# Kernel tuning notes

Measured on AMD Instinct MI355X. Metric: run time of the kernel, lower is better.

Reference implementation:

```python
import jax, jax.numpy as jnp
import numpy as np

N_AC = 8192     # number of amacrine cells
N_BC = 8192     # number of bipolar-cell helpers
T_KERNEL = 52   # len(torch.arange(0.8, 0, -1/64)) with input_frequency=64


def setup_inputs() -> dict:
    key = jax.random.key(0)
    k_x, k_w, k_k, k_s, k_o = jax.random.split(key, 5)
    x = jax.random.normal(k_x, (N_BC, T_KERNEL), dtype=jnp.float32)
    bc_ac_weight = jax.random.normal(k_w, (N_AC, N_BC), dtype=jnp.float32) / np.sqrt(N_BC)
    ac_kernel = jax.random.normal(k_k, (N_AC, T_KERNEL), dtype=jnp.float32)
    # normalize kernel rows like compute_ac_kernel does
    ac_kernel = ac_kernel / jnp.linalg.norm(ac_kernel, axis=1, keepdims=True)
    # slopes come from exp(log_slope) in the original -> keep positive
    ac_sigmoid_slope = jax.random.uniform(k_s, (N_AC,), dtype=jnp.float32) + 0.5
    ac_sigmoid_offset = 0.1 * jax.random.normal(k_o, (N_AC,), dtype=jnp.float32)
    return {
        "x": x,
        "bc_ac_weight": bc_ac_weight,
        "ac_kernel": ac_kernel,
        "ac_sigmoid_slope": ac_sigmoid_slope,
        "ac_sigmoid_offset": ac_sigmoid_offset,
    }


def reference(x, bc_ac_weight, ac_kernel, ac_sigmoid_slope, ac_sigmoid_offset):
    """One AC feedback step.

    x:                (nBC, T)   BC activity history window
    bc_ac_weight:     (nAC, nBC) precomputed (exp of log weights)
    ac_kernel:        (nAC, T)   precomputed normalized double-exp kernel
    ac_sigmoid_slope: (nAC,)
    ac_sigmoid_offset:(nAC,)
    returns:          (nAC,)
    """
    t_kernel = ac_kernel.shape[-1]
    y = bc_ac_weight @ x  # (nAC, T)
    if y.shape[-1] < t_kernel:  # static-shape left zero-pad as in F.pad
        y = jnp.pad(y, ((0, 0), (t_kernel - y.shape[-1], 0)))
    s = jnp.sum(ac_kernel * y, axis=1)  # temporal weighted sum -> (nAC,)
    # precomputed_sigmoid: sigmoid with per-cell slope and offset
    return jax.nn.sigmoid(ac_sigmoid_slope * (s - ac_sigmoid_offset))
```

## Files before the change

### kernel.cpp

```cpp
#include <hip/hip_runtime.h>
#include <hip/hip_bf16.h>
#include <math.h>

#define N_AC  8192
#define N_BC  8192
#define T_K   52
#define T_PAD 64

typedef __bf16 bf16x8 __attribute__((ext_vector_type(8)));
typedef float  f32x4  __attribute__((ext_vector_type(4)));

__global__ void xpose_kernel(const float* __restrict__ x, __bf16* __restrict__ xT) {
    int b = blockIdx.x * blockDim.x + threadIdx.x;
    if (b >= N_BC) return;
    #pragma unroll
    for (int t = 0; t < T_PAD; ++t) {
        float v = (t < T_K) ? x[b * T_K + t] : 0.0f;
        xT[(size_t)t * N_BC + b] = (__bf16)v;
    }
}

__global__ __launch_bounds__(256) void ac_feedback_kernel(
    const float*  __restrict__ W,
    const __bf16* __restrict__ xT,
    const float*  __restrict__ kern,
    const float*  __restrict__ slope,
    const float*  __restrict__ offs,
    float*        __restrict__ out)
{
    const int lane = threadIdx.x & 63;
    const int wave = threadIdx.x >> 6;
    const int quad = lane >> 4;
    const int l15  = lane & 15;
    const int a0   = blockIdx.x * 16;

    const float* wrow = W + (size_t)(a0 + l15) * N_BC;

    f32x4 acc[4] = {};

    const int kseg = N_BC / 4;
    const int kbeg = wave * kseg;
    const int koff = quad * 8;

    #pragma unroll 4
    for (int k = kbeg; k < kbeg + kseg; k += 32) {
        const float* wp = wrow + k + koff;
        float4 w0 = *(const float4*)(wp);
        float4 w1 = *(const float4*)(wp + 4);
        bf16x8 af;
        af[0] = (__bf16)w0.x; af[1] = (__bf16)w0.y;
        af[2] = (__bf16)w0.z; af[3] = (__bf16)w0.w;
        af[4] = (__bf16)w1.x; af[5] = (__bf16)w1.y;
        af[6] = (__bf16)w1.z; af[7] = (__bf16)w1.w;
        #pragma unroll
        for (int nt = 0; nt < 4; ++nt) {
            bf16x8 bf = *(const bf16x8*)(xT + (size_t)(nt * 16 + l15) * N_BC + k + koff);
            acc[nt] = __builtin_amdgcn_mfma_f32_16x16x32_bf16(af, bf, acc[nt], 0, 0, 0);
        }
    }

    float p[4] = {0.f, 0.f, 0.f, 0.f};
    #pragma unroll
    for (int nt = 0; nt < 4; ++nt) {
        int t = nt * 16 + l15;
        if (t < T_K) {
            #pragma unroll
            for (int r = 0; r < 4; ++r) {
                int grow = a0 + quad * 4 + r;
                p[r] += acc[nt][r] * kern[grow * T_K + t];
            }
        }
    }

    #pragma unroll
    for (int m = 1; m <= 8; m <<= 1) {
        #pragma unroll
        for (int r = 0; r < 4; ++r) p[r] += __shfl_xor(p[r], m);
    }

    __shared__ float red[4][16];
    if (l15 == 0) {
        #pragma unroll
        for (int r = 0; r < 4; ++r) red[wave][quad * 4 + r] = p[r];
    }
    __syncthreads();

    if (threadIdx.x < 16) {
        int a = a0 + threadIdx.x;
        float s = red[0][threadIdx.x] + red[1][threadIdx.x]
                + red[2][threadIdx.x] + red[3][threadIdx.x];
        float z = slope[a] * (s - offs[a]);
        out[a] = 1.0f / (1.0f + __expf(-z));
    }
}

extern "C" void kernel_launch(void* const* d_in, const int* in_sizes, int n_in,
                              void* d_out, int out_size, void* d_ws, size_t ws_size,
                              hipStream_t stream) {
    const float* x     = (const float*)d_in[0];
    const float* W     = (const float*)d_in[1];
    const float* kern  = (const float*)d_in[2];
    const float* slope = (const float*)d_in[3];
    const float* offs  = (const float*)d_in[4];
    float* out = (float*)d_out;

    __bf16* xT = (__bf16*)d_ws;

    xpose_kernel<<<dim3(N_BC / 256), dim3(256), 0, stream>>>(x, xT);
    ac_feedback_kernel<<<dim3(N_AC / 16), dim3(256), 0, stream>>>(
        W, xT, kern, slope, offs, out);
}
```

Baseline: 397.5 us.

## Split K across blocks and stage W tiles through LDS with coalesced loads

The GEMM kernel now uses a 2D grid that splits the reduction dimension into four segments, one per block. Each block loads 16x512 tiles of W with fully coalesced float4 loads, converts them to bf16, and stores them in padded shared memory before running the MFMAs. Partial sums go to a workspace buffer, and a new final kernel adds them and applies the sigmoid. This aims to improve W streaming coalescing and raise block-level parallelism, at the cost of an extra launch, a partials buffer, and barriers with no double buffering.

Result: slower. 433.7 us (+9.1%).

```diff
diff --git a/kernel.cpp b/kernel.cpp
--- a/kernel.cpp
+++ b/kernel.cpp
@@ -7,7 +7,14 @@
 #define T_K   52
 #define T_PAD 64
 
+#define KSPLIT 4
+#define KSEG   (N_BC / KSPLIT)
+#define BK     512
+#define NCHUNK (KSEG / BK)
+#define LDS_STRIDE 520
+
 typedef __bf16 bf16x8 __attribute__((ext_vector_type(8)));
+typedef __bf16 bf16x4 __attribute__((ext_vector_type(4)));
 typedef float  f32x4  __attribute__((ext_vector_type(4)));
 
 __global__ void xpose_kernel(const float* __restrict__ x, __bf16* __restrict__ xT) {
@@ -20,43 +27,54 @@
     }
 }
 
-__global__ __launch_bounds__(256) void ac_feedback_kernel(
+__global__ __launch_bounds__(256) void ac_gemm_kernel(
     const float*  __restrict__ W,
     const __bf16* __restrict__ xT,
     const float*  __restrict__ kern,
-    const float*  __restrict__ slope,
-    const float*  __restrict__ offs,
-    float*        __restrict__ out)
+    float*        __restrict__ partials)
 {
-    const int lane = threadIdx.x & 63;
-    const int wave = threadIdx.x >> 6;
+    const int tid  = threadIdx.x;
+    const int lane = tid & 63;
+    const int wave = tid >> 6;
     const int quad = lane >> 4;
     const int l15  = lane & 15;
     const int a0   = blockIdx.x * 16;
+    const int kbase = blockIdx.y * KSEG;
 
-    const float* wrow = W + (size_t)(a0 + l15) * N_BC;
+    __shared__ __bf16 As[16 * LDS_STRIDE];
 
     f32x4 acc[4] = {};
 
-    const int kseg = N_BC / 4;
-    const int kbeg = wave * kseg;
     const int koff = quad * 8;
+    const int ks   = wave * (BK / 4);
 
-    #pragma unroll 4
-    for (int k = kbeg; k < kbeg + kseg; k += 32) {
-        const float* wp = wrow + k + koff;
-        float4 w0 = *(const float4*)(wp);
-        float4 w1 = *(const float4*)(wp + 4);
-        bf16x8 af;
-        af[0] = (__bf16)w0.x; af[1] = (__bf16)w0.y;
-        af[2] = (__bf16)w0.z; af[3] = (__bf16)w0.w;
-        af[4] = (__bf16)w1.x; af[5] = (__bf16)w1.y;
-        af[6] = (__bf16)w1.z; af[7] = (__bf16)w1.w;
+    for (int c = 0; c < NCHUNK; ++c) {
+        const int kc = kbase + c * BK;
+
         #pragma unroll
-        for (int nt = 0; nt < 4; ++nt) {
-            bf16x8 bf = *(const bf16x8*)(xT + (size_t)(nt * 16 + l15) * N_BC + k + koff);
-            acc[nt] = __builtin_amdgcn_mfma_f32_16x16x32_bf16(af, bf, acc[nt], 0, 0, 0);
+        for (int j = 0; j < 8; ++j) {
+            int idx4 = j * 256 + tid;
+            int row  = idx4 >> 7;
+            int col  = (idx4 & 127) << 2;
+            float4 f = *(const float4*)(W + (size_t)(a0 + row) * N_BC + kc + col);
+            bf16x4 h;
+            h[0] = (__bf16)f.x; h[1] = (__bf16)f.y;
+            h[2] = (__bf16)f.z; h[3] = (__bf16)f.w;
+            *(bf16x4*)&As[row * LDS_STRIDE + col] = h;
         }
+        __syncthreads();
+
+        #pragma unroll
+        for (int s = 0; s < 4; ++s) {
+            int kk = ks + s * 32 + koff;
+            bf16x8 af = *(const bf16x8*)&As[l15 * LDS_STRIDE + kk];
+            #pragma unroll
+            for (int nt = 0; nt < 4; ++nt) {
+                bf16x8 bf = *(const bf16x8*)(xT + (size_t)(nt * 16 + l15) * N_BC + kc + kk);
+                acc[nt] = __builtin_amdgcn_mfma_f32_16x16x32_bf16(af, bf, acc[nt], 0, 0, 0);
+            }
+        }
+        __syncthreads();
     }
 
     float p[4] = {0.f, 0.f, 0.f, 0.f};
@@ -71,7 +89,6 @@
             }
         }
     }
-
     #pragma unroll
     for (int m = 1; m <= 8; m <<= 1) {
         #pragma unroll
@@ -85,13 +102,22 @@
     }
     __syncthreads();
 
-    if (threadIdx.x < 16) {
-        int a = a0 + threadIdx.x;
-        float s = red[0][threadIdx.x] + red[1][threadIdx.x]
-                + red[2][threadIdx.x] + red[3][threadIdx.x];
-        float z = slope[a] * (s - offs[a]);
-        out[a] = 1.0f / (1.0f + __expf(-z));
+    if (tid < 16) {
+        float s = red[0][tid] + red[1][tid] + red[2][tid] + red[3][tid];
+        partials[blockIdx.y * N_AC + a0 + tid] = s;
     }
+}
+
+__global__ void ac_final_kernel(const float* __restrict__ partials,
+                                const float* __restrict__ slope,
+                                const float* __restrict__ offs,
+                                float* __restrict__ out) {
+    int a = blockIdx.x * blockDim.x + threadIdx.x;
+    if (a >= N_AC) return;
+    float s = partials[a] + partials[N_AC + a]
+            + partials[2 * N_AC + a] + partials[3 * N_AC + a];
+    float z = slope[a] * (s - offs[a]);
+    out[a] = 1.0f / (1.0f + __expf(-z));
 }
 
 extern "C" void kernel_launch(void* const* d_in, const int* in_sizes, int n_in,
@@ -104,9 +130,12 @@
     const float* offs  = (const float*)d_in[4];
     float* out = (float*)d_out;
 
-    __bf16* xT = (__bf16*)d_ws;
+    __bf16* xT      = (__bf16*)d_ws;
+    float* partials = (float*)((char*)d_ws + (size_t)T_PAD * N_BC * sizeof(__bf16));
 
     xpose_kernel<<<dim3(N_BC / 256), dim3(256), 0, stream>>>(x, xT);
-    ac_feedback_kernel<<<dim3(N_AC / 16), dim3(256), 0, stream>>>(
-        W, xT, kern, slope, offs, out);
+    ac_gemm_kernel<<<dim3(N_AC / 16, KSPLIT), dim3(256), 0, stream>>>(
+        W, xT, kern, partials);
+    ac_final_kernel<<<dim3(N_AC / 256), dim3(256), 0, stream>>>(
+        partials, slope, offs, out);
 }
```

## Split GEMM K dimension across blocks with separate reduction kernel and parallel transpose

Applied to the files above, without the earlier changes.

The K reduction is split across 4 blocks per AC tile (16 K-slices), giving 2048 blocks instead of 512. Each slice writes its partial temporal-weighted sum to a workspace buffer, and a third kernel sums the partials and applies the sigmoid. The transpose kernel now uses one thread per output element, so stores are coalesced. The cost is an extra launch, a partials round trip through memory, and re-reading the kernel weights in every slice.

Result: slower. 410.3 us (+3.2%).

```diff
diff --git a/kernel.cpp b/kernel.cpp
--- a/kernel.cpp
+++ b/kernel.cpp
@@ -7,43 +7,42 @@
 #define T_K   52
 #define T_PAD 64
 
+#define KSPLIT 16
+#define KSEG   (N_BC / KSPLIT)
+
 typedef __bf16 bf16x8 __attribute__((ext_vector_type(8)));
 typedef float  f32x4  __attribute__((ext_vector_type(4)));
 
 __global__ void xpose_kernel(const float* __restrict__ x, __bf16* __restrict__ xT) {
-    int b = blockIdx.x * blockDim.x + threadIdx.x;
-    if (b >= N_BC) return;
-    #pragma unroll
-    for (int t = 0; t < T_PAD; ++t) {
-        float v = (t < T_K) ? x[b * T_K + t] : 0.0f;
-        xT[(size_t)t * N_BC + b] = (__bf16)v;
-    }
+    int gt = blockIdx.x * blockDim.x + threadIdx.x;
+    int b = gt & (N_BC - 1);
+    int t = gt >> 13;
+    float v = (t < T_K) ? x[b * T_K + t] : 0.0f;
+    xT[gt] = (__bf16)v;
 }
 
-__global__ __launch_bounds__(256) void ac_feedback_kernel(
+__global__ __launch_bounds__(256) void ac_gemm_kernel(
     const float*  __restrict__ W,
     const __bf16* __restrict__ xT,
     const float*  __restrict__ kern,
-    const float*  __restrict__ slope,
-    const float*  __restrict__ offs,
-    float*        __restrict__ out)
+    float*        __restrict__ partials)
 {
-    const int lane = threadIdx.x & 63;
-    const int wave = threadIdx.x >> 6;
+    const int tid  = threadIdx.x;
+    const int lane = tid & 63;
+    const int wave = tid >> 6;
     const int quad = lane >> 4;
     const int l15  = lane & 15;
     const int a0   = blockIdx.x * 16;
+    const int ksub = blockIdx.y * 4 + wave;
+    const int kbeg = ksub * KSEG;
 
     const float* wrow = W + (size_t)(a0 + l15) * N_BC;
+    const int koff = quad * 8;
 
     f32x4 acc[4] = {};
 
-    const int kseg = N_BC / 4;
-    const int kbeg = wave * kseg;
-    const int koff = quad * 8;
-
-    #pragma unroll 4
-    for (int k = kbeg; k < kbeg + kseg; k += 32) {
+    #pragma unroll 2
+    for (int k = kbeg; k < kbeg + KSEG; k += 32) {
         const float* wp = wrow + k + koff;
         float4 w0 = *(const float4*)(wp);
         float4 w1 = *(const float4*)(wp + 4);
@@ -71,27 +70,30 @@
             }
         }
     }
-
     #pragma unroll
     for (int m = 1; m <= 8; m <<= 1) {
         #pragma unroll
         for (int r = 0; r < 4; ++r) p[r] += __shfl_xor(p[r], m);
     }
 
-    __shared__ float red[4][16];
     if (l15 == 0) {
         #pragma unroll
-        for (int r = 0; r < 4; ++r) red[wave][quad * 4 + r] = p[r];
+        for (int r = 0; r < 4; ++r)
+            partials[ksub * N_AC + a0 + quad * 4 + r] = p[r];
     }
-    __syncthreads();
+}
 
-    if (threadIdx.x < 16) {
-        int a = a0 + threadIdx.x;
-        float s = red[0][threadIdx.x] + red[1][threadIdx.x]
-                + red[2][threadIdx.x] + red[3][threadIdx.x];
-        float z = slope[a] * (s - offs[a]);
-        out[a] = 1.0f / (1.0f + __expf(-z));
-    }
+__global__ void ac_final_kernel(const float* __restrict__ partials,
+                                const float* __restrict__ slope,
+                                const float* __restrict__ offs,
+                                float* __restrict__ out) {
+    int a = blockIdx.x * blockDim.x + threadIdx.x;
+    if (a >= N_AC) return;
+    float s = 0.f;
+    #pragma unroll
+    for (int ks = 0; ks < KSPLIT; ++ks) s += partials[ks * N_AC + a];
+    float z = slope[a] * (s - offs[a]);
+    out[a] = 1.0f / (1.0f + __expf(-z));
 }
 
 extern "C" void kernel_launch(void* const* d_in, const int* in_sizes, int n_in,
@@ -104,9 +106,12 @@
     const float* offs  = (const float*)d_in[4];
     float* out = (float*)d_out;
 
-    __bf16* xT = (__bf16*)d_ws;
+    __bf16* xT      = (__bf16*)d_ws;
+    float* partials = (float*)((char*)d_ws + (size_t)T_PAD * N_BC * sizeof(__bf16));
 
-    xpose_kernel<<<dim3(N_BC / 256), dim3(256), 0, stream>>>(x, xT);
-    ac_feedback_kernel<<<dim3(N_AC / 16), dim3(256), 0, stream>>>(
-        W, xT, kern, slope, offs, out);
+    xpose_kernel<<<dim3(T_PAD * N_BC / 256), dim3(256), 0, stream>>>(x, xT);
+    ac_gemm_kernel<<<dim3(N_AC / 16, KSPLIT / 4), dim3(256), 0, stream>>>(
+        W, xT, kern, partials);
+    ac_final_kernel<<<dim3(N_AC / 256), dim3(256), 0, stream>>>(
+        partials, slope, offs, out);
 }
```
